# Performance work log

Measured on AMD Instinct MI355X. Metric: run time of the kernel, lower is better.

## Reference

```python
import jax, jax.numpy as jnp
import numpy as np

B, S, D, H = 2, 2048, 768, 12
DH = D // H  # 64


def setup_inputs() -> dict:
    key = jax.random.key(0)
    ks = jax.random.split(key, 8)
    std = 1.0 / np.sqrt(D)
    return {
        "q": jax.random.normal(ks[0], (B, S, D), dtype=jnp.float32),
        "k": jax.random.normal(ks[1], (B, S, D), dtype=jnp.float32),
        "v": jax.random.normal(ks[2], (B, S, D), dtype=jnp.float32),
        "Wq": jax.random.normal(ks[3], (D, D), dtype=jnp.float32) * std,
        "bq": jnp.zeros((D,), dtype=jnp.float32),
        "Wk": jax.random.normal(ks[4], (D, D), dtype=jnp.float32) * std,
        "bk": jnp.zeros((D,), dtype=jnp.float32),
        "Wv": jax.random.normal(ks[5], (D, D), dtype=jnp.float32) * std,
        "bv": jnp.zeros((D,), dtype=jnp.float32),
        "Wo": jax.random.normal(ks[6], (D, D), dtype=jnp.float32) * std,
        "bo": jnp.zeros((D,), dtype=jnp.float32),
    }


def reference(q, k, v, Wq, bq, Wk, bk, Wv, bv, Wo, bo):
    b, s, d = q.shape
    # linear projections then split heads: [b, s, d] -> [b, h, s, dh]
    def split(x):
        return x.reshape(b, s, H, DH).transpose(0, 2, 1, 3)

    qh = split(q @ Wq + bq)
    kh = split(k @ Wk + bk)
    vh = split(v @ Wv + bv)

    scale = 1.0 / jnp.sqrt(jnp.asarray(DH, dtype=q.dtype))
    # full [b, h, s, s] score matrix (faithful to the original unfused op)
    scores = jnp.einsum("bhqd,bhkd->bhqk", qh, kh) * scale
    # look-ahead mask: 1 above the diagonal, added as mask * -1e9
    look_ahead = jnp.triu(jnp.ones((s, s), dtype=scores.dtype), k=1)
    scores = scores + look_ahead * (-1e9)

    attn = jax.nn.softmax(scores, axis=-1)  # dropout is identity at inference
    ctx = jnp.einsum("bhqk,bhkd->bhqd", attn, vh)
    ctx = ctx.transpose(0, 2, 1, 3).reshape(b, s, d)
    return ctx @ Wo + bo
```

## Files before the change

kernel.cpp:

```cpp
#include <hip/hip_runtime.h>
#include <hip/hip_bf16.h>
#include <stdint.h>

#define Bz 2
#define Sz 2048
#define Dz 768
#define Hz 12
#define DHz 64
#define Mz (Bz*Sz)
#define NQT16 128

typedef __attribute__((ext_vector_type(4))) float f32x4;
typedef __attribute__((ext_vector_type(8))) short bf16x8;
typedef unsigned short u16;
typedef __attribute__((ext_vector_type(8))) unsigned short u16x8;

__device__ __forceinline__ u16 f2bf(float f) {
  union { float f; uint32_t u; } c; c.f = f;
  uint32_t u = c.u;
  return (u16)((u + 0x7fffu + ((u >> 16) & 1u)) >> 16);
}

#define GLL16(gsrc, ldst) \
  __builtin_amdgcn_global_load_lds((const __attribute__((address_space(1))) void*)(gsrc), \
                                   (__attribute__((address_space(3))) void*)(ldst), 16, 0, 0)

__device__ __forceinline__ f32x4 mfma16(bf16x8 a, bf16x8 b, f32x4 c) {
  return __builtin_amdgcn_mfma_f32_16x16x32_bf16(a, b, c, 0, 0, 0);
}

__global__ void cvt3_kernel(const float* __restrict__ qa, const float* __restrict__ ka,
                            const float* __restrict__ va,
                            u16* __restrict__ qo, u16* __restrict__ ko, u16* __restrict__ vo,
                            int n8) {
  int i = blockIdx.x * blockDim.x + threadIdx.x;
  if (i >= n8) return;
  int z = blockIdx.y;
  const float* src = (z == 0) ? qa : (z == 1) ? ka : va;
  u16* dst = (z == 0) ? qo : (z == 1) ? ko : vo;
  const float4* s4 = (const float4*)src;
  float4 a = s4[(size_t)i * 2];
  float4 b = s4[(size_t)i * 2 + 1];
  u16x8 o;
  o[0] = f2bf(a.x); o[1] = f2bf(a.y); o[2] = f2bf(a.z); o[3] = f2bf(a.w);
  o[4] = f2bf(b.x); o[5] = f2bf(b.y); o[6] = f2bf(b.z); o[7] = f2bf(b.w);
  *(u16x8*)(dst + (size_t)i * 8) = o;
}

__global__ void wtrans4_kernel(const float* __restrict__ W0, const float* __restrict__ W1,
                               const float* __restrict__ W2, const float* __restrict__ W3,
                               u16* __restrict__ T0, u16* __restrict__ T1,
                               u16* __restrict__ T2, u16* __restrict__ T3) {
  __shared__ float tile[32][33];
  int z = blockIdx.z;
  const float* W = (z == 0) ? W0 : (z == 1) ? W1 : (z == 2) ? W2 : W3;
  u16* Wt = (z == 0) ? T0 : (z == 1) ? T1 : (z == 2) ? T2 : T3;
  int bx = blockIdx.x * 32, by = blockIdx.y * 32;
  int tx = threadIdx.x & 31, ty = threadIdx.x >> 5;
#pragma unroll
  for (int i = 0; i < 32; i += 8)
    tile[ty + i][tx] = W[(size_t)(by + ty + i) * Dz + bx + tx];
  __syncthreads();
#pragma unroll
  for (int i = 0; i < 32; i += 8)
    Wt[(size_t)(bx + ty + i) * Dz + by + tx] = f2bf(tile[tx][ty + i]);
}

__device__ __forceinline__ void gemm_core(
    const u16* __restrict__ A, const u16* __restrict__ Wt,
    const float* __restrict__ bias, void* __restrict__ out, int mode, float oscale,
    u16 (*As)[128 * 32], u16 (*Bs)[128 * 32])
{
  const int tid = threadIdx.x;
  const int wid = tid >> 6, lane = tid & 63;
  const int wm = wid >> 1, wn = wid & 1;
  const int m0 = blockIdx.x * 128, n0 = blockIdx.y * 128;
  const int fq = lane >> 4, fr = lane & 15;

  int aoff[2];
#pragma unroll
  for (int c = 0; c < 2; ++c) {
    int off  = (wid * 2 + c) * 1024 + lane * 16;
    int row  = off >> 6;
    int colb = (off & 63) ^ (((row >> 1) & 3) << 4);
    aoff[c]  = row * Dz + (colb >> 1);
  }

  int raddr[4], rbaddr[4];
#pragma unroll
  for (int f = 0; f < 4; ++f) {
    int rowA = wm * 64 + f * 16 + fr;
    raddr[f]  = rowA * 64 + ((fq * 16) ^ (((rowA >> 1) & 3) << 4));
    int rowB = wn * 64 + f * 16 + fr;
    rbaddr[f] = rowB * 64 + ((fq * 16) ^ (((rowB >> 1) & 3) << 4));
  }

  f32x4 acc[4][4];
  const f32x4 zero = {0.f, 0.f, 0.f, 0.f};
#pragma unroll
  for (int i = 0; i < 4; ++i)
#pragma unroll
    for (int j = 0; j < 4; ++j) acc[i][j] = zero;

  const u16* Abase = A + (size_t)m0 * Dz;
  const u16* Bbase = Wt + (size_t)n0 * Dz;

  const int NKT = Dz / 32;
#pragma unroll
  for (int c = 0; c < 2; ++c) {
    GLL16(Abase + aoff[c], (char*)As[0] + (wid * 2 + c) * 1024);
    GLL16(Bbase + aoff[c], (char*)Bs[0] + (wid * 2 + c) * 1024);
  }
  int cur = 0;

  for (int kt = 0; kt < NKT; ++kt) {
    int nx = cur + 1; if (nx == 3) nx = 0;
    if (kt + 1 < NKT) {
      int ke = (kt + 1) * 32;
#pragma unroll
      for (int c = 0; c < 2; ++c) {
        GLL16(Abase + ke + aoff[c], (char*)As[nx] + (wid * 2 + c) * 1024);
        GLL16(Bbase + ke + aoff[c], (char*)Bs[nx] + (wid * 2 + c) * 1024);
      }
      asm volatile("s_waitcnt vmcnt(4)" ::: "memory");
    } else {
      asm volatile("s_waitcnt vmcnt(0)" ::: "memory");
    }
    __builtin_amdgcn_s_barrier();
    __builtin_amdgcn_sched_barrier(0);

    bf16x8 af[4], bf[4];
#pragma unroll
    for (int f = 0; f < 4; ++f) {
      af[f] = *(const bf16x8*)((const char*)As[cur] + raddr[f]);
      bf[f] = *(const bf16x8*)((const char*)Bs[cur] + rbaddr[f]);
    }
    __builtin_amdgcn_s_setprio(1);
#pragma unroll
    for (int i = 0; i < 4; ++i)
#pragma unroll
      for (int j = 0; j < 4; ++j)
        acc[i][j] = mfma16(af[i], bf[j], acc[i][j]);
    __builtin_amdgcn_s_setprio(0);
    cur = nx;
  }

  if (mode == 2) {
    float* O = (float*)out;
#pragma unroll
    for (int i = 0; i < 4; ++i) {
      int grow = m0 + wm * 64 + i * 16 + fq * 4;
#pragma unroll
      for (int j = 0; j < 4; ++j) {
        int gcol = n0 + wn * 64 + j * 16 + fr;
        float bv = bias[gcol];
#pragma unroll
        for (int r = 0; r < 4; ++r)
          O[(size_t)(grow + r) * Dz + gcol] = acc[i][j][r] + bv;
      }
    }
  } else {
    u16* O = (u16*)out;
#pragma unroll
    for (int i = 0; i < 4; ++i) {
      int grow = m0 + wm * 64 + i * 16 + fq * 4;
#pragma unroll
      for (int j = 0; j < 4; ++j) {
        int gcol = n0 + wn * 64 + j * 16 + fr;
        float bv = bias[gcol];
        int h = gcol >> 6, dh = gcol & 63;
#pragma unroll
        for (int r = 0; r < 4; ++r) {
          int t = grow + r;
          int b = t >> 11, s = t & 2047;
          int bh = b * Hz + h;
          u16 val = f2bf((acc[i][j][r] + bv) * oscale);
          size_t idx;
          if (mode == 0) {
            idx = ((((size_t)bh * 128 + (s >> 4)) * 2 + (dh >> 5)) * 64
                   + ((dh >> 3) & 3) * 16 + (s & 15)) * 8 + (dh & 7);
          } else if (mode == 3) {
            idx = (((((size_t)bh * 32 + (s >> 6)) * 4 + ((s >> 4) & 3)) * 2 + (dh >> 5)) * 64
                   + ((dh >> 3) & 3) * 16 + (s & 15)) * 8 + (dh & 7);
          } else {
            idx = (((((size_t)bh * 32 + (s >> 6)) * 4 + (dh >> 4)) * 2 + ((s >> 5) & 1)) * 64
                   + ((s >> 3) & 3) * 16 + (dh & 15)) * 8 + (s & 7);
          }
          O[idx] = val;
        }
      }
    }
  }
}

#define QSCALE 0.1803368801111404f

__global__ __launch_bounds__(256, 2) void gemm_qkv(
    const u16* __restrict__ qb, const u16* __restrict__ kb, const u16* __restrict__ vb,
    const u16* __restrict__ Wqt, const u16* __restrict__ Wkt, const u16* __restrict__ Wvt,
    const float* __restrict__ bq, const float* __restrict__ bk, const float* __restrict__ bv,
    u16* __restrict__ Qf, u16* __restrict__ Kf, u16* __restrict__ Vf)
{
  __shared__ u16 As[3][128 * 32];
  __shared__ u16 Bs[3][128 * 32];
  const u16* A; const u16* W; const float* bias; u16* out; int mode; float osc;
  if (blockIdx.z == 0)      { A = qb; W = Wqt; bias = bq; out = Qf; mode = 0; osc = QSCALE; }
  else if (blockIdx.z == 1) { A = kb; W = Wkt; bias = bk; out = Kf; mode = 3; osc = 1.f; }
  else                      { A = vb; W = Wvt; bias = bv; out = Vf; mode = 1; osc = 1.f; }
  gemm_core(A, W, bias, out, mode, osc, As, Bs);
}

__global__ __launch_bounds__(256, 2) void gemm_out_k(
    const u16* __restrict__ ctx, const u16* __restrict__ Wot,
    const float* __restrict__ bo, float* __restrict__ out)
{
  __shared__ u16 As[3][128 * 32];
  __shared__ u16 Bs[3][128 * 32];
  gemm_core(ctx, Wot, bo, (void*)out, 2, 1.f, As, Bs);
}

__global__ __launch_bounds__(128, 2) void attn_kernel(
    const u16* __restrict__ Qf, const u16* __restrict__ Kf,
    const u16* __restrict__ Vf, u16* __restrict__ ctx)
{
  __shared__ u16 Ps[2][16 * 64];
  __shared__ float o1buf[64 * 16];
  __shared__ float ml1[2][16];
  const int tid = threadIdx.x, wid = tid >> 6, lane = tid & 63;
  const int fq = lane >> 4, fr = lane & 15;
  const int bh = blockIdx.x;
  const int qt = (NQT16 - 1) - blockIdx.y;
  const int b = bh / Hz, h = bh % Hz;
  const int qbase = qt * 16;
  const int nkt = (qbase + 79) >> 6;

  const bf16x8* Qf8 = (const bf16x8*)Qf + (size_t)bh * 128 * 2 * 64;
  const bf16x8* Kf8 = (const bf16x8*)Kf + (size_t)bh * 32 * 8 * 64;
  const bf16x8* Vf8 = (const bf16x8*)Vf + (size_t)bh * 32 * 8 * 64;

  bf16x8 aq[2];
#pragma unroll
  for (int kk = 0; kk < 2; ++kk)
    aq[kk] = Qf8[((size_t)qt * 2 + kk) * 64 + lane];

  const f32x4 zero = {0.f, 0.f, 0.f, 0.f};
  f32x4 o[4];
#pragma unroll
  for (int i = 0; i < 4; ++i) o[i] = zero;
  float m_r[4], l_r[4];
#pragma unroll
  for (int r = 0; r < 4; ++r) { m_r[r] = -1e30f; l_r[r] = 0.f; }

  char* Pw = (char*)Ps[wid];

  if (wid < nkt) {
    bf16x8 kfr[4][2], vfr[4][2];
#pragma unroll
    for (int j = 0; j < 4; ++j)
#pragma unroll
      for (int kk = 0; kk < 2; ++kk)
        kfr[j][kk] = Kf8[((size_t)wid * 8 + j * 2 + kk) * 64 + lane];

    for (int kt = wid; kt < nkt; kt += 2) {
#pragma unroll
      for (int fo = 0; fo < 4; ++fo)
#pragma unroll
        for (int kk = 0; kk < 2; ++kk)
          vfr[fo][kk] = Vf8[((size_t)kt * 8 + fo * 2 + kk) * 64 + lane];

      f32x4 s[4];
#pragma unroll
      for (int j = 0; j < 4; ++j) s[j] = zero;
      __builtin_amdgcn_s_setprio(1);
#pragma unroll
      for (int j = 0; j < 4; ++j)
#pragma unroll
        for (int kk = 0; kk < 2; ++kk)
          s[j] = mfma16(aq[kk], kfr[j][kk], s[j]);
      __builtin_amdgcn_s_setprio(0);

      if (kt + 2 < nkt) {
#pragma unroll
        for (int j = 0; j < 4; ++j)
#pragma unroll
          for (int kk = 0; kk < 2; ++kk)
            kfr[j][kk] = Kf8[((size_t)(kt + 2) * 8 + j * 2 + kk) * 64 + lane];
      }

      if (kt == nkt - 1) {
#pragma unroll
        for (int j = 0; j < 4; ++j) {
          int keyg = kt * 64 + j * 16 + fr;
#pragma unroll
          for (int r = 0; r < 4; ++r)
            if (keyg > qbase + fq * 4 + r) s[j][r] = -1e30f;
        }
      }

      float mt[4];
#pragma unroll
      for (int r = 0; r < 4; ++r) mt[r] = s[0][r];
#pragma unroll
      for (int j = 1; j < 4; ++j)
#pragma unroll
        for (int r = 0; r < 4; ++r) mt[r] = fmaxf(mt[r], s[j][r]);

      int nd = 0;
#pragma unroll
      for (int r = 0; r < 4; ++r) nd |= (mt[r] > m_r[r] + 8.f) ? 1 : 0;
      if (__any(nd)) {
#pragma unroll
        for (int msk = 1; msk < 16; msk <<= 1)
#pragma unroll
          for (int r = 0; r < 4; ++r) mt[r] = fmaxf(mt[r], __shfl_xor(mt[r], msk));
#pragma unroll
        for (int r = 0; r < 4; ++r) {
          float mn = fmaxf(m_r[r], mt[r]);
          float alpha = __builtin_amdgcn_exp2f(m_r[r] - mn);
          m_r[r] = mn;
          l_r[r] *= alpha;
#pragma unroll
          for (int i = 0; i < 4; ++i) o[i][r] *= alpha;
        }
      }

#pragma unroll
      for (int j = 0; j < 4; ++j) {
#pragma unroll
        for (int r = 0; r < 4; ++r) {
          float e = __builtin_amdgcn_exp2f(s[j][r] - m_r[r]);
          l_r[r] += e;
          int qr = fq * 4 + r;
          int key2 = (j * 16 + fr) * 2;
          *(u16*)(Pw + qr * 128 + (key2 ^ ((qr & 7) << 4))) = f2bf(e);
        }
      }

      __builtin_amdgcn_s_setprio(1);
#pragma unroll
      for (int kk = 0; kk < 2; ++kk) {
        int cbP = (kk * 64 + fq * 16) ^ ((fr & 7) << 4);
        bf16x8 pa = *(const bf16x8*)(Pw + fr * 128 + cbP);
#pragma unroll
        for (int fo = 0; fo < 4; ++fo)
          o[fo] = mfma16(pa, vfr[fo][kk], o[fo]);
      }
      __builtin_amdgcn_s_setprio(0);
    }
  }

#pragma unroll
  for (int msk = 1; msk < 16; msk <<= 1)
#pragma unroll
    for (int r = 0; r < 4; ++r) l_r[r] += __shfl_xor(l_r[r], msk);

  if (wid == 1) {
#pragma unroll
    for (int fo = 0; fo < 4; ++fo)
#pragma unroll
      for (int r = 0; r < 4; ++r)
        o1buf[lane * 16 + fo * 4 + r] = o[fo][r];
    if (fr == 0) {
#pragma unroll
      for (int r = 0; r < 4; ++r) {
        ml1[0][fq * 4 + r] = m_r[r];
        ml1[1][fq * 4 + r] = l_r[r];
      }
    }
  }
  __syncthreads();

  if (wid == 0) {
    float a0[4], a1[4], li[4];
#pragma unroll
    for (int r = 0; r < 4; ++r) {
      float m1 = ml1[0][fq * 4 + r];
      float l1 = ml1[1][fq * 4 + r];
      float mm = fmaxf(m_r[r], m1);
      a0[r] = __builtin_amdgcn_exp2f(m_r[r] - mm);
      a1[r] = __builtin_amdgcn_exp2f(m1 - mm);
      li[r] = 1.0f / (l_r[r] * a0[r] + l1 * a1[r]);
    }
#pragma unroll
    for (int fo = 0; fo < 4; ++fo) {
      int dh = fo * 16 + fr;
#pragma unroll
      for (int r = 0; r < 4; ++r) {
        float o1 = o1buf[lane * 16 + fo * 4 + r];
        float val = (o[fo][r] * a0[r] + o1 * a1[r]) * li[r];
        int qg = qbase + fq * 4 + r;
        ctx[((size_t)b * Sz + qg) * Dz + h * DHz + dh] = f2bf(val);
      }
    }
  }
}

extern "C" void kernel_launch(void* const* d_in, const int* in_sizes, int n_in,
                              void* d_out, int out_size, void* d_ws, size_t ws_size,
                              hipStream_t stream) {
  const float* q  = (const float*)d_in[0];
  const float* k  = (const float*)d_in[1];
  const float* v  = (const float*)d_in[2];
  const float* Wq = (const float*)d_in[3];
  const float* bq = (const float*)d_in[4];
  const float* Wk = (const float*)d_in[5];
  const float* bk = (const float*)d_in[6];
  const float* Wv = (const float*)d_in[7];
  const float* bv = (const float*)d_in[8];
  const float* Wo = (const float*)d_in[9];
  const float* bo = (const float*)d_in[10];
  float* out = (float*)d_out;

  char* ws = (char*)d_ws;
  size_t off = 0;
  auto alloc = [&](size_t bytes) {
    void* p = ws + off;
    off += (bytes + 255) & ~(size_t)255;
    return p;
  };
  u16* qb  = (u16*)alloc((size_t)Mz * Dz * 2);
  u16* kb  = (u16*)alloc((size_t)Mz * Dz * 2);
  u16* vb  = (u16*)alloc((size_t)Mz * Dz * 2);
  u16* Wqt = (u16*)alloc((size_t)Dz * Dz * 2);
  u16* Wkt = (u16*)alloc((size_t)Dz * Dz * 2);
  u16* Wvt = (u16*)alloc((size_t)Dz * Dz * 2);
  u16* Wot = (u16*)alloc((size_t)Dz * Dz * 2);
  u16* Qf  = (u16*)alloc((size_t)Bz * Hz * Sz * DHz * 2);
  u16* Kf  = (u16*)alloc((size_t)Bz * Hz * Sz * DHz * 2);
  u16* Vf  = (u16*)alloc((size_t)Bz * Hz * Sz * DHz * 2);
  u16* ctx = (u16*)alloc((size_t)Mz * Dz * 2);

  int n8 = Mz * Dz / 8;
  int cblk = (n8 + 255) / 256;
  cvt3_kernel<<<dim3(cblk, 3), 256, 0, stream>>>(q, k, v, qb, kb, vb, n8);

  wtrans4_kernel<<<dim3(Dz / 32, Dz / 32, 4), 256, 0, stream>>>(
      Wq, Wk, Wv, Wo, Wqt, Wkt, Wvt, Wot);

  gemm_qkv<<<dim3(Mz / 128, Dz / 128, 3), 256, 0, stream>>>(
      qb, kb, vb, Wqt, Wkt, Wvt, bq, bk, bv, Qf, Kf, Vf);

  attn_kernel<<<dim3(Bz * Hz, NQT16), 128, 0, stream>>>(Qf, Kf, Vf, ctx);

  gemm_out_k<<<dim3(Mz / 128, Dz / 128), 256, 0, stream>>>(ctx, Wot, bo, out);
}
```

Before: 93.18 us.

## Merge prep kernels, use 64-row tiles for output GEMM, raise occupancy bounds

Merges the activation bf16 conversion and the weight transpose into one prep kernel launch, which removes one launch. Adds a dedicated output-projection GEMM with 64x128 tiles, doubling the block count from 192 to 384 so the device's CUs are better filled, and gives it a larger launch_bounds occupancy hint. Also raises the QKV GEMM occupancy hint from 2 to 3 blocks per CU. This risks register spills under the tighter bounds, and smaller tiles mean less data reuse per block.

```diff
diff --git a/kernel.cpp b/kernel.cpp
--- a/kernel.cpp
+++ b/kernel.cpp
@@ -29,41 +29,46 @@
   return __builtin_amdgcn_mfma_f32_16x16x32_bf16(a, b, c, 0, 0, 0);
 }
 
-__global__ void cvt3_kernel(const float* __restrict__ qa, const float* __restrict__ ka,
-                            const float* __restrict__ va,
-                            u16* __restrict__ qo, u16* __restrict__ ko, u16* __restrict__ vo,
-                            int n8) {
-  int i = blockIdx.x * blockDim.x + threadIdx.x;
-  if (i >= n8) return;
-  int z = blockIdx.y;
-  const float* src = (z == 0) ? qa : (z == 1) ? ka : va;
-  u16* dst = (z == 0) ? qo : (z == 1) ? ko : vo;
-  const float4* s4 = (const float4*)src;
-  float4 a = s4[(size_t)i * 2];
-  float4 b = s4[(size_t)i * 2 + 1];
-  u16x8 o;
-  o[0] = f2bf(a.x); o[1] = f2bf(a.y); o[2] = f2bf(a.z); o[3] = f2bf(a.w);
-  o[4] = f2bf(b.x); o[5] = f2bf(b.y); o[6] = f2bf(b.z); o[7] = f2bf(b.w);
-  *(u16x8*)(dst + (size_t)i * 8) = o;
-}
-
-__global__ void wtrans4_kernel(const float* __restrict__ W0, const float* __restrict__ W1,
-                               const float* __restrict__ W2, const float* __restrict__ W3,
-                               u16* __restrict__ T0, u16* __restrict__ T1,
-                               u16* __restrict__ T2, u16* __restrict__ T3) {
+#define CVTB 1536
+__global__ __launch_bounds__(256) void prep_kernel(
+    const float* __restrict__ qa, const float* __restrict__ ka, const float* __restrict__ va,
+    u16* __restrict__ qo, u16* __restrict__ ko, u16* __restrict__ vo,
+    const float* __restrict__ W0, const float* __restrict__ W1,
+    const float* __restrict__ W2, const float* __restrict__ W3,
+    u16* __restrict__ T0, u16* __restrict__ T1,
+    u16* __restrict__ T2, u16* __restrict__ T3)
+{
   __shared__ float tile[32][33];
-  int z = blockIdx.z;
-  const float* W = (z == 0) ? W0 : (z == 1) ? W1 : (z == 2) ? W2 : W3;
-  u16* Wt = (z == 0) ? T0 : (z == 1) ? T1 : (z == 2) ? T2 : T3;
-  int bx = blockIdx.x * 32, by = blockIdx.y * 32;
-  int tx = threadIdx.x & 31, ty = threadIdx.x >> 5;
-#pragma unroll
-  for (int i = 0; i < 32; i += 8)
-    tile[ty + i][tx] = W[(size_t)(by + ty + i) * Dz + bx + tx];
-  __syncthreads();
-#pragma unroll
-  for (int i = 0; i < 32; i += 8)
-    Wt[(size_t)(bx + ty + i) * Dz + by + tx] = f2bf(tile[tx][ty + i]);
+  int bid = blockIdx.x;
+  if (bid < 3 * CVTB) {
+    int z = bid / CVTB;
+    int i = (bid % CVTB) * 256 + threadIdx.x;
+    const float* src = (z == 0) ? qa : (z == 1) ? ka : va;
+    u16* dst = (z == 0) ? qo : (z == 1) ? ko : vo;
+    const float4* s4 = (const float4*)src;
+    float4 a = s4[(size_t)i * 2];
+    float4 b = s4[(size_t)i * 2 + 1];
+    u16x8 o;
+    o[0] = f2bf(a.x); o[1] = f2bf(a.y); o[2] = f2bf(a.z); o[3] = f2bf(a.w);
+    o[4] = f2bf(b.x); o[5] = f2bf(b.y); o[6] = f2bf(b.z); o[7] = f2bf(b.w);
+    *(u16x8*)(dst + (size_t)i * 8) = o;
+  } else {
+    int w = bid - 3 * CVTB;
+    int z = w / 576;
+    int rem = w - z * 576;
+    int by = rem / 24, bxi = rem - by * 24;
+    const float* W = (z == 0) ? W0 : (z == 1) ? W1 : (z == 2) ? W2 : W3;
+    u16* Wt = (z == 0) ? T0 : (z == 1) ? T1 : (z == 2) ? T2 : T3;
+    int bx = bxi * 32, byy = by * 32;
+    int tx = threadIdx.x & 31, ty = threadIdx.x >> 5;
+#pragma unroll
+    for (int i = 0; i < 32; i += 8)
+      tile[ty + i][tx] = W[(size_t)(byy + ty + i) * Dz + bx + tx];
+    __syncthreads();
+#pragma unroll
+    for (int i = 0; i < 32; i += 8)
+      Wt[(size_t)(bx + ty + i) * Dz + byy + tx] = f2bf(tile[tx][ty + i]);
+  }
 }
 
 __device__ __forceinline__ void gemm_core(
@@ -145,21 +150,7 @@
     cur = nx;
   }
 
-  if (mode == 2) {
-    float* O = (float*)out;
-#pragma unroll
-    for (int i = 0; i < 4; ++i) {
-      int grow = m0 + wm * 64 + i * 16 + fq * 4;
-#pragma unroll
-      for (int j = 0; j < 4; ++j) {
-        int gcol = n0 + wn * 64 + j * 16 + fr;
-        float bv = bias[gcol];
-#pragma unroll
-        for (int r = 0; r < 4; ++r)
-          O[(size_t)(grow + r) * Dz + gcol] = acc[i][j][r] + bv;
-      }
-    }
-  } else {
+  {
     u16* O = (u16*)out;
 #pragma unroll
     for (int i = 0; i < 4; ++i) {
@@ -193,9 +184,111 @@
   }
 }
 
+__device__ __forceinline__ void gemm_out_core64(
+    const u16* __restrict__ A, const u16* __restrict__ Wt,
+    const float* __restrict__ bias, float* __restrict__ O,
+    u16 (*As)[64 * 32], u16 (*Bs)[128 * 32])
+{
+  const int tid = threadIdx.x;
+  const int wid = tid >> 6, lane = tid & 63;
+  const int wm = wid >> 1, wn = wid & 1;
+  const int m0 = blockIdx.x * 64, n0 = blockIdx.y * 128;
+  const int fq = lane >> 4, fr = lane & 15;
+
+  int aoff;
+  {
+    int off  = tid * 16;
+    int row  = off >> 6;
+    int colb = (off & 63) ^ (((row >> 1) & 3) << 4);
+    aoff = row * Dz + (colb >> 1);
+  }
+  int boff[2];
+#pragma unroll
+  for (int c = 0; c < 2; ++c) {
+    int off  = tid * 16 + c * 4096;
+    int row  = off >> 6;
+    int colb = (off & 63) ^ (((row >> 1) & 3) << 4);
+    boff[c] = row * Dz + (colb >> 1);
+  }
+
+  int raddr[2], rbaddr[4];
+#pragma unroll
+  for (int f = 0; f < 2; ++f) {
+    int rowA = wm * 32 + f * 16 + fr;
+    raddr[f] = rowA * 64 + ((fq * 16) ^ (((rowA >> 1) & 3) << 4));
+  }
+#pragma unroll
+  for (int f = 0; f < 4; ++f) {
+    int rowB = wn * 64 + f * 16 + fr;
+    rbaddr[f] = rowB * 64 + ((fq * 16) ^ (((rowB >> 1) & 3) << 4));
+  }
+
+  f32x4 acc[2][4];
+  const f32x4 zero = {0.f, 0.f, 0.f, 0.f};
+#pragma unroll
+  for (int i = 0; i < 2; ++i)
+#pragma unroll
+    for (int j = 0; j < 4; ++j) acc[i][j] = zero;
+
+  const u16* Abase = A + (size_t)m0 * Dz;
+  const u16* Bbase = Wt + (size_t)n0 * Dz;
+
+  const int NKT = Dz / 32;
+  GLL16(Abase + aoff, (char*)As[0] + tid * 16);
+#pragma unroll
+  for (int c = 0; c < 2; ++c)
+    GLL16(Bbase + boff[c], (char*)Bs[0] + tid * 16 + c * 4096);
+  int cur = 0;
+
+  for (int kt = 0; kt < NKT; ++kt) {
+    int nx = cur + 1; if (nx == 3) nx = 0;
+    if (kt + 1 < NKT) {
+      int ke = (kt + 1) * 32;
+      GLL16(Abase + ke + aoff, (char*)As[nx] + tid * 16);
+#pragma unroll
+      for (int c = 0; c < 2; ++c)
+        GLL16(Bbase + ke + boff[c], (char*)Bs[nx] + tid * 16 + c * 4096);
+      asm volatile("s_waitcnt vmcnt(3)" ::: "memory");
+    } else {
+      asm volatile("s_waitcnt vmcnt(0)" ::: "memory");
+    }
+    __builtin_amdgcn_s_barrier();
+    __builtin_amdgcn_sched_barrier(0);
+
+    bf16x8 af[2], bf[4];
+#pragma unroll
+    for (int f = 0; f < 2; ++f)
+      af[f] = *(const bf16x8*)((const char*)As[cur] + raddr[f]);
+#pragma unroll
+    for (int f = 0; f < 4; ++f)
+      bf[f] = *(const bf16x8*)((const char*)Bs[cur] + rbaddr[f]);
+    __builtin_amdgcn_s_setprio(1);
+#pragma unroll
+    for (int i = 0; i < 2; ++i)
+#pragma unroll
+      for (int j = 0; j < 4; ++j)
+        acc[i][j] = mfma16(af[i], bf[j], acc[i][j]);
+    __builtin_amdgcn_s_setprio(0);
+    cur = nx;
+  }
+
+#pragma unroll
+  for (int i = 0; i < 2; ++i) {
+    int grow = m0 + wm * 32 + i * 16 + fq * 4;
+#pragma unroll
+    for (int j = 0; j < 4; ++j) {
+      int gcol = n0 + wn * 64 + j * 16 + fr;
+      float bv = bias[gcol];
+#pragma unroll
+      for (int r = 0; r < 4; ++r)
+        O[(size_t)(grow + r) * Dz + gcol] = acc[i][j][r] + bv;
+    }
+  }
+}
+
 #define QSCALE 0.1803368801111404f
 
-__global__ __launch_bounds__(256, 2) void gemm_qkv(
+__global__ __launch_bounds__(256, 3) void gemm_qkv(
     const u16* __restrict__ qb, const u16* __restrict__ kb, const u16* __restrict__ vb,
     const u16* __restrict__ Wqt, const u16* __restrict__ Wkt, const u16* __restrict__ Wvt,
     const float* __restrict__ bq, const float* __restrict__ bk, const float* __restrict__ bv,
@@ -210,13 +303,13 @@
   gemm_core(A, W, bias, out, mode, osc, As, Bs);
 }
 
-__global__ __launch_bounds__(256, 2) void gemm_out_k(
+__global__ __launch_bounds__(256, 4) void gemm_out_k(
     const u16* __restrict__ ctx, const u16* __restrict__ Wot,
     const float* __restrict__ bo, float* __restrict__ out)
 {
-  __shared__ u16 As[3][128 * 32];
+  __shared__ u16 As[3][64 * 32];
   __shared__ u16 Bs[3][128 * 32];
-  gemm_core(ctx, Wot, bo, (void*)out, 2, 1.f, As, Bs);
+  gemm_out_core64(ctx, Wot, bo, out, As, Bs);
 }
 
 __global__ __launch_bounds__(128, 2) void attn_kernel(
@@ -430,17 +523,13 @@
   u16* Vf  = (u16*)alloc((size_t)Bz * Hz * Sz * DHz * 2);
   u16* ctx = (u16*)alloc((size_t)Mz * Dz * 2);
 
-  int n8 = Mz * Dz / 8;
-  int cblk = (n8 + 255) / 256;
-  cvt3_kernel<<<dim3(cblk, 3), 256, 0, stream>>>(q, k, v, qb, kb, vb, n8);
-
-  wtrans4_kernel<<<dim3(Dz / 32, Dz / 32, 4), 256, 0, stream>>>(
-      Wq, Wk, Wv, Wo, Wqt, Wkt, Wvt, Wot);
+  prep_kernel<<<3 * CVTB + 4 * 576, 256, 0, stream>>>(
+      q, k, v, qb, kb, vb, Wq, Wk, Wv, Wo, Wqt, Wkt, Wvt, Wot);
 
   gemm_qkv<<<dim3(Mz / 128, Dz / 128, 3), 256, 0, stream>>>(
       qb, kb, vb, Wqt, Wkt, Wvt, bq, bk, bv, Qf, Kf, Vf);
 
   attn_kernel<<<dim3(Bz * Hz, NQT16), 128, 0, stream>>>(Qf, Kf, Vf, ctx);
 
-  gemm_out_k<<<dim3(Mz / 128, Dz / 128), 256, 0, stream>>>(ctx, Wot, bo, out);
-}
+  gemm_out_k<<<dim3(Mz / 64, Dz / 128), 256, 0, stream>>>(ctx, Wot, bo, out);
+}
```

New measurement: 88.80 us, median of 2. 4.7% less time.
